# Kernel optimization log

Hardware: AMD Instinct MI355X
Metric: run time of the kernel (lower is better)

Reference implementation:

```python
import jax, jax.numpy as jnp
import numpy as np

H, W = 512, 512
G = 8192
ALPHA_THRESH = 1.0 / 255.0        # meta_f32[0]
TRANS_THRESH = 1.0e-4             # meta_f32[1]
ALPHA_CAP = 0.99                  # meta_f32[6]
BG = jnp.zeros((3,), dtype=jnp.float32)  # config.background


def setup_inputs() -> dict:
    key = jax.random.key(0)
    ks = jax.random.split(key, 7)
    mx = jax.random.uniform(ks[0], (G,), minval=0.0, maxval=float(W))
    my = jax.random.uniform(ks[1], (G,), minval=0.0, maxval=float(H))
    means2d = jnp.stack([mx, my], axis=-1)
    # Build valid conics (inverse 2x2 covariances) from random rotation + scales
    theta = jax.random.uniform(ks[2], (G,), minval=0.0, maxval=2.0 * np.pi)
    s = jax.random.uniform(ks[3], (G, 2), minval=2.0, maxval=12.0)  # px stddevs
    ct, st = jnp.cos(theta), jnp.sin(theta)
    v1, v2 = s[:, 0] ** 2, s[:, 1] ** 2
    ca = ct * ct * v1 + st * st * v2
    cb = ct * st * (v1 - v2)
    cc = st * st * v1 + ct * ct * v2
    det = ca * cc - cb * cb
    conics = jnp.stack([cc / det, -cb / det, ca / det], axis=-1)  # [G,3] = (a,b,c)
    colors = jax.random.uniform(ks[4], (G, 3))
    opacities = jax.random.uniform(ks[5], (G,))
    depths = jax.random.uniform(ks[6], (G,), minval=0.1, maxval=100.0)
    return {"means2d": means2d, "conics": conics, "colors": colors,
            "opacities": opacities, "depths": depths}


def reference(means2d, conics, colors, opacities, depths):
    # Stable front-to-back depth sort (mirrors perm = argsort(depths, stable))
    perm = jnp.argsort(depths, stable=True)
    m = means2d[perm]
    cn = conics[perm]
    col = colors[perm]
    op = opacities[perm]
    a, b, c = cn[:, 0], cn[:, 1], cn[:, 2]
    px = jnp.arange(W, dtype=means2d.dtype) + 0.5  # pixel centers

    def row(y):
        py = y.astype(means2d.dtype) + 0.5
        dx = px[:, None] - m[None, :, 0]          # [W,G]
        dy = py - m[:, 1]                          # [G]
        sigma = 0.5 * (a * dx * dx + c * dy * dy) + b * dx * dy  # [W,G]
        alpha = jnp.minimum(ALPHA_CAP, op * jnp.exp(-sigma))
        alpha = jnp.where((sigma < 0) | (alpha < ALPHA_THRESH), 0.0, alpha)
        # exclusive cumulative transmittance along depth order
        Tprev = jnp.cumprod(1.0 - alpha, axis=-1)
        Tprev = jnp.concatenate([jnp.ones((W, 1), alpha.dtype), Tprev[:, :-1]], axis=-1)
        # early-termination: splats seen after T drops below threshold contribute 0
        wgt = alpha * Tprev * (Tprev >= TRANS_THRESH)  # [W,G]
        rgb = wgt @ col                                 # [W,3]
        t_rem = 1.0 - wgt.sum(axis=-1)                  # remaining transmittance
        return rgb + t_rem[:, None] * BG

    return jax.lax.map(row, jnp.arange(H))  # [H,W,3]
```

## Files before the change

### kernel.cpp

```cpp
#include <hip/hip_runtime.h>

#define G 8192
#define IMG_W 512
#define IMG_H 512
#define TILE 16
#define NTX (IMG_W / TILE)
#define NTY (IMG_H / TILE)
#define BLK 256
#define CAP 1024
#define ALPHA_THRESH (1.0f/255.0f)
#define ALPHA_CAP 0.99f
#define TRANS_THRESH 1e-4f

__global__ __launch_bounds__(BLK)
void range_kernel(const float* __restrict__ means2d,
                  const float* __restrict__ conics,
                  const float* __restrict__ opac,
                  unsigned int* __restrict__ ranges)
{
    int g = blockIdx.x * BLK + threadIdx.x;
    if (g >= G) return;
    float op = opac[g];
    unsigned int packed = 0xFFu;
    if (op * 255.0f >= 1.0f) {
        float smax = __logf(op * 255.0f);
        float a = conics[3*g], b = conics[3*g+1], c = conics[3*g+2];
        float det = fmaxf(a * c - b * b, 1e-12f);
        float rx = sqrtf(fmaxf(2.0f * smax * c / det, 0.0f)) * 1.0001f + 0.01f;
        float ry = sqrtf(fmaxf(2.0f * smax * a / det, 0.0f)) * 1.0001f + 0.01f;
        float mx = means2d[2*g], my = means2d[2*g+1];
        int txmin = (int)ceilf ((mx - rx - 15.5f) * 0.0625f);
        int txmax = (int)floorf((mx + rx -  0.5f) * 0.0625f);
        int tymin = (int)ceilf ((my - ry - 15.5f) * 0.0625f);
        int tymax = (int)floorf((my + ry -  0.5f) * 0.0625f);
        if (!(txmax < 0 || txmin > NTX-1 || tymax < 0 || tymin > NTY-1 ||
              txmin > txmax || tymin > tymax)) {
            txmin = max(txmin, 0); txmax = min(txmax, NTX-1);
            tymin = max(tymin, 0); tymax = min(tymax, NTY-1);
            packed = (unsigned)txmin | ((unsigned)txmax << 8)
                   | ((unsigned)tymin << 16) | ((unsigned)tymax << 24);
        }
    }
    ranges[g] = packed;
}

__device__ __forceinline__ int hitp(unsigned p, unsigned btx, unsigned bty)
{
    return (btx >= (p & 0xffu)) & (btx <= ((p >> 8) & 0xffu)) &
           (bty >= ((p >> 16) & 0xffu)) & (bty <= (p >> 24));
}

__global__ __launch_bounds__(BLK)
void tile_kernel(const unsigned int* __restrict__ ranges,
                 const float* __restrict__ depths,
                 const float* __restrict__ means2d,
                 const float* __restrict__ conics,
                 const float* __restrict__ colors,
                 const float* __restrict__ opac,
                 float*       __restrict__ out)
{
    __shared__ unsigned short slist[CAP];
    __shared__ unsigned long long keys[CAP];
    __shared__ int woff[4];
    __shared__ float smx[BLK], smy[BLK], sa[BLK], sb[BLK], sc[BLK];
    __shared__ float sr[BLK], sg[BLK], sbl[BLK], sop[BLK];

    const int tx = threadIdx.x, ty = threadIdx.y;
    const int t = ty * TILE + tx;
    const int lane = t & 63, w = t >> 6;
    const unsigned btx = blockIdx.x, bty = blockIdx.y;

    const uint4* r4 = (const uint4*)ranges;
    const int wbase = w * (G / 4);
    uint4 rv[8];
    #pragma unroll
    for (int i = 0; i < 8; ++i)
        rv[i] = r4[(wbase >> 2) + i * 64 + lane];

    int cnt = 0;
    #pragma unroll
    for (int i = 0; i < 8; ++i)
        cnt += hitp(rv[i].x, btx, bty) + hitp(rv[i].y, btx, bty)
             + hitp(rv[i].z, btx, bty) + hitp(rv[i].w, btx, bty);
    #pragma unroll
    for (int d = 1; d < 64; d <<= 1) cnt += __shfl_xor(cnt, d);
    if (lane == 0) woff[w] = cnt;
    __syncthreads();

    int offs = 0;
    for (int ww = 0; ww < w; ++ww) offs += woff[ww];
    const int N = min(woff[0] + woff[1] + woff[2] + woff[3], CAP);

    const unsigned long long lt = (1ull << lane) - 1ull;
    #pragma unroll
    for (int i = 0; i < 8; ++i) {
        int gbase = wbase + i * 256 + lane * 4;
        int h0 = hitp(rv[i].x, btx, bty), h1 = hitp(rv[i].y, btx, bty);
        int h2 = hitp(rv[i].z, btx, bty), h3 = hitp(rv[i].w, btx, bty);
        unsigned long long m0 = __ballot(h0), m1 = __ballot(h1);
        unsigned long long m2 = __ballot(h2), m3 = __ballot(h3);
        int pos = offs + __popcll(m0 & lt) + __popcll(m1 & lt)
                       + __popcll(m2 & lt) + __popcll(m3 & lt);
        if (h0) { if (pos < CAP) slist[pos] = (unsigned short)(gbase    ); pos++; }
        if (h1) { if (pos < CAP) slist[pos] = (unsigned short)(gbase + 1); pos++; }
        if (h2) { if (pos < CAP) slist[pos] = (unsigned short)(gbase + 2); pos++; }
        if (h3) { if (pos < CAP) slist[pos] = (unsigned short)(gbase + 3); pos++; }
        offs += __popcll(m0) + __popcll(m1) + __popcll(m2) + __popcll(m3);
    }
    __syncthreads();

    for (int i = t; i < N; i += BLK) {
        unsigned idx = slist[i];
        keys[i] = ((unsigned long long)__float_as_uint(depths[idx]) << 13)
                | (unsigned long long)idx;
    }
    __syncthreads();
    for (int i = t; i < N; i += BLK) {
        unsigned long long ke = keys[i];
        int r = 0;
        #pragma unroll 4
        for (int j = 0; j < N; ++j) r += (keys[j] < ke);
        slist[r] = (unsigned short)(ke & 0x1fffull);
    }
    __syncthreads();

    const float px = (float)(blockIdx.x * TILE + tx) + 0.5f;
    const float py = (float)(blockIdx.y * TILE + ty) + 0.5f;
    float T = 1.0f, accr = 0.0f, accg = 0.0f, accb = 0.0f;
    bool done = false;

    for (int base = 0; base < N; base += BLK) {
        int n = min(BLK, N - base);
        if (t < n) {
            int idx = slist[base + t];
            smx[t] = means2d[2*idx];
            smy[t] = means2d[2*idx + 1];
            sa [t] = conics[3*idx];
            sb [t] = conics[3*idx + 1];
            sc [t] = conics[3*idx + 2];
            sr [t] = colors[3*idx];
            sg [t] = colors[3*idx + 1];
            sbl[t] = colors[3*idx + 2];
            sop[t] = opac[idx];
        }
        __syncthreads();
        if (!done) {
            for (int i = 0; i < n; ++i) {
                float dx = px - smx[i];
                float dy = py - smy[i];
                float sigma = 0.5f * (sa[i]*dx*dx + sc[i]*dy*dy) + sb[i]*dx*dy;
                float al = sop[i] * __expf(-sigma);
                bool ok = (sigma >= 0.0f) && (al >= ALPHA_THRESH);
                al = ok ? fminf(al, ALPHA_CAP) : 0.0f;
                float wgt = al * T;
                accr = fmaf(wgt, sr[i],  accr);
                accg = fmaf(wgt, sg[i],  accg);
                accb = fmaf(wgt, sbl[i], accb);
                T *= (1.0f - al);
                if (T < TRANS_THRESH) { done = true; break; }
            }
        }
        if (__syncthreads_and((int)done)) break;
    }

    const int o = ((blockIdx.y * TILE + ty) * IMG_W + blockIdx.x * TILE + tx) * 3;
    out[o]     = accr;
    out[o + 1] = accg;
    out[o + 2] = accb;
}

extern "C" void kernel_launch(void* const* d_in, const int* in_sizes, int n_in,
                              void* d_out, int out_size, void* d_ws, size_t ws_size,
                              hipStream_t stream)
{
    const float* means2d = (const float*)d_in[0];
    const float* conics  = (const float*)d_in[1];
    const float* colors  = (const float*)d_in[2];
    const float* opac    = (const float*)d_in[3];
    const float* depths  = (const float*)d_in[4];
    float* out = (float*)d_out;
    unsigned int* ranges = (unsigned int*)d_ws;

    range_kernel<<<G / BLK, BLK, 0, stream>>>(means2d, conics, opac, ranges);
    tile_kernel<<<dim3(NTX, NTY), dim3(TILE, TILE), 0, stream>>>(
        ranges, depths, means2d, conics, colors, opac, out);
}
```

Before: 93.83 us.

## Stage splat parameters in wave registers and broadcast via readlane instead of LDS

Each 64-lane wave now loads a chunk of 64 sorted splats into per-lane registers and broadcasts each one to the whole wave with readlane. This replaces the block-wide shared-memory staging and its per-batch __syncthreads. The next chunk is prefetched while the current one is composited, and waves terminate on their own once no lane has transmittance above threshold, checked every 8 splats. The thread-to-pixel mapping changes to a 1D block of four 16x4 wave strips, and the conic is pre-halved so sigma is computed with FMAs. In exchange, individual pixels no longer stop exactly when their own transmittance drops, which adds negligible extra contributions, and register pressure rises from the double-buffered splat parameters.

```diff
diff --git a/kernel.cpp b/kernel.cpp
--- a/kernel.cpp
+++ b/kernel.cpp
@@ -50,6 +50,11 @@
            (bty >= ((p >> 16) & 0xffu)) & (bty <= (p >> 24));
 }
 
+__device__ __forceinline__ float rdl(float v, int l)
+{
+    return __int_as_float(__builtin_amdgcn_readlane(__float_as_int(v), l));
+}
+
 __global__ __launch_bounds__(BLK)
 void tile_kernel(const unsigned int* __restrict__ ranges,
                  const float* __restrict__ depths,
@@ -62,11 +67,8 @@
     __shared__ unsigned short slist[CAP];
     __shared__ unsigned long long keys[CAP];
     __shared__ int woff[4];
-    __shared__ float smx[BLK], smy[BLK], sa[BLK], sb[BLK], sc[BLK];
-    __shared__ float sr[BLK], sg[BLK], sbl[BLK], sop[BLK];
-
-    const int tx = threadIdx.x, ty = threadIdx.y;
-    const int t = ty * TILE + tx;
+
+    const int t = threadIdx.x;
     const int lane = t & 63, w = t >> 6;
     const unsigned btx = blockIdx.x, bty = blockIdx.y;
 
@@ -124,46 +126,68 @@
     }
     __syncthreads();
 
-    const float px = (float)(blockIdx.x * TILE + tx) + 0.5f;
-    const float py = (float)(blockIdx.y * TILE + ty) + 0.5f;
+    const float px = (float)(btx * TILE + (lane & 15)) + 0.5f;
+    const float py = (float)(bty * TILE + w * 4 + (lane >> 4)) + 0.5f;
+
     float T = 1.0f, accr = 0.0f, accg = 0.0f, accb = 0.0f;
-    bool done = false;
-
-    for (int base = 0; base < N; base += BLK) {
-        int n = min(BLK, N - base);
-        if (t < n) {
-            int idx = slist[base + t];
-            smx[t] = means2d[2*idx];
-            smy[t] = means2d[2*idx + 1];
-            sa [t] = conics[3*idx];
-            sb [t] = conics[3*idx + 1];
-            sc [t] = conics[3*idx + 2];
-            sr [t] = colors[3*idx];
-            sg [t] = colors[3*idx + 1];
-            sbl[t] = colors[3*idx + 2];
-            sop[t] = opac[idx];
+    const int nchunk = (N + 63) >> 6;
+
+    float cmx, cmy, ca2, cb, cc2, cop, cr, cg, cbl;
+    float nmx, nmy, na2, nb, nc2, nop, nr, ng, nbl;
+
+    auto fetch = [&](int c, float& mx, float& my, float& a2, float& b,
+                     float& c2, float& op, float& r, float& g, float& bl) {
+        int pos = (c << 6) + lane;
+        if (pos < N) {
+            int idx = slist[pos];
+            mx = means2d[2*idx];      my = means2d[2*idx + 1];
+            float a = conics[3*idx];  b  = conics[3*idx + 1];
+            float cc = conics[3*idx + 2];
+            a2 = 0.5f * a;            c2 = 0.5f * cc;
+            r  = colors[3*idx];       g  = colors[3*idx + 1];
+            bl = colors[3*idx + 2];   op = opac[idx];
+        } else {
+            mx = 0.f; my = 0.f; a2 = 0.f; b = 0.f; c2 = 0.f;
+            op = 0.f; r = 0.f; g = 0.f; bl = 0.f;
         }
-        __syncthreads();
-        if (!done) {
-            for (int i = 0; i < n; ++i) {
-                float dx = px - smx[i];
-                float dy = py - smy[i];
-                float sigma = 0.5f * (sa[i]*dx*dx + sc[i]*dy*dy) + sb[i]*dx*dy;
-                float al = sop[i] * __expf(-sigma);
+    };
+
+    if (nchunk > 0)
+        fetch(0, cmx, cmy, ca2, cb, cc2, cop, cr, cg, cbl);
+
+    bool alive = true;
+    for (int c = 0; c < nchunk && alive; ++c) {
+        if (c + 1 < nchunk)
+            fetch(c + 1, nmx, nmy, na2, nb, nc2, nop, nr, ng, nbl);
+        for (int j = 0; j < 64; j += 8) {
+            #pragma unroll
+            for (int u = 0; u < 8; ++u) {
+                int l = j + u;
+                float mx = rdl(cmx, l), my = rdl(cmy, l);
+                float a2 = rdl(ca2, l), b  = rdl(cb, l), c2 = rdl(cc2, l);
+                float op = rdl(cop, l), r  = rdl(cr, l), g  = rdl(cg, l);
+                float bl = rdl(cbl, l);
+                float dx = px - mx;
+                float dy = py - my;
+                float sigma = fmaf(fmaf(a2, dx, b * dy), dx, c2 * dy * dy);
+                float al = op * __expf(-sigma);
                 bool ok = (sigma >= 0.0f) && (al >= ALPHA_THRESH);
                 al = ok ? fminf(al, ALPHA_CAP) : 0.0f;
                 float wgt = al * T;
-                accr = fmaf(wgt, sr[i],  accr);
-                accg = fmaf(wgt, sg[i],  accg);
-                accb = fmaf(wgt, sbl[i], accb);
+                accr = fmaf(wgt, r,  accr);
+                accg = fmaf(wgt, g,  accg);
+                accb = fmaf(wgt, bl, accb);
                 T *= (1.0f - al);
-                if (T < TRANS_THRESH) { done = true; break; }
             }
+            if (!__any(T >= TRANS_THRESH)) { alive = false; break; }
         }
-        if (__syncthreads_and((int)done)) break;
-    }
-
-    const int o = ((blockIdx.y * TILE + ty) * IMG_W + blockIdx.x * TILE + tx) * 3;
+        cmx = nmx; cmy = nmy; ca2 = na2; cb = nb; cc2 = nc2;
+        cop = nop; cr = nr; cg = ng; cbl = nbl;
+    }
+
+    const int x = btx * TILE + (lane & 15);
+    const int y = bty * TILE + w * 4 + (lane >> 4);
+    const int o = (y * IMG_W + x) * 3;
     out[o]     = accr;
     out[o + 1] = accg;
     out[o + 2] = accb;
@@ -182,6 +206,6 @@
     unsigned int* ranges = (unsigned int*)d_ws;
 
     range_kernel<<<G / BLK, BLK, 0, stream>>>(means2d, conics, opac, ranges);
-    tile_kernel<<<dim3(NTX, NTY), dim3(TILE, TILE), 0, stream>>>(
+    tile_kernel<<<dim3(NTX, NTY), BLK, 0, stream>>>(
         ranges, depths, means2d, conics, colors, opac, out);
 }
```

After: 106.6 us. +13.6%, slower.

## Composite two pixels per thread with packed float4 splat data in LDS

Applied to the files above, without the earlier changes.

Halves the tile block to 128 threads, with each thread rendering two pixels eight rows apart so every splat read from shared memory and the dx terms are reused. Splat attributes are packed into two float4 (pre-halved conics, fp16 red/green) to cut LDS traffic. Early termination becomes a wavefront-wide check every eight splats instead of per pixel. Risks: a slower rank sort with fewer threads, fp16 colour rounding, and slightly more accumulation past the transmittance threshold.

```diff
diff --git a/kernel.cpp b/kernel.cpp
--- a/kernel.cpp
+++ b/kernel.cpp
@@ -1,4 +1,5 @@
 #include <hip/hip_runtime.h>
+#include <hip/hip_fp16.h>
 
 #define G 8192
 #define IMG_W 512
@@ -7,6 +8,7 @@
 #define NTX (IMG_W / TILE)
 #define NTY (IMG_H / TILE)
 #define BLK 256
+#define BLK2 128
 #define CAP 1024
 #define ALPHA_THRESH (1.0f/255.0f)
 #define ALPHA_CAP 0.99f
@@ -50,7 +52,7 @@
            (bty >= ((p >> 16) & 0xffu)) & (bty <= (p >> 24));
 }
 
-__global__ __launch_bounds__(BLK)
+__global__ __launch_bounds__(BLK2)
 void tile_kernel(const unsigned int* __restrict__ ranges,
                  const float* __restrict__ depths,
                  const float* __restrict__ means2d,
@@ -61,42 +63,38 @@
 {
     __shared__ unsigned short slist[CAP];
     __shared__ unsigned long long keys[CAP];
-    __shared__ int woff[4];
-    __shared__ float smx[BLK], smy[BLK], sa[BLK], sb[BLK], sc[BLK];
-    __shared__ float sr[BLK], sg[BLK], sbl[BLK], sop[BLK];
-
-    const int tx = threadIdx.x, ty = threadIdx.y;
-    const int t = ty * TILE + tx;
+    __shared__ int woff[2];
+    __shared__ float4 buf[BLK2 * 2];
+
+    const int t = threadIdx.x;
     const int lane = t & 63, w = t >> 6;
     const unsigned btx = blockIdx.x, bty = blockIdx.y;
 
     const uint4* r4 = (const uint4*)ranges;
-    const int wbase = w * (G / 4);
-    uint4 rv[8];
-    #pragma unroll
-    for (int i = 0; i < 8; ++i)
-        rv[i] = r4[(wbase >> 2) + i * 64 + lane];
+    const int wq = w * (4096 / 4);
 
     int cnt = 0;
-    #pragma unroll
-    for (int i = 0; i < 8; ++i)
-        cnt += hitp(rv[i].x, btx, bty) + hitp(rv[i].y, btx, bty)
-             + hitp(rv[i].z, btx, bty) + hitp(rv[i].w, btx, bty);
+    #pragma unroll 4
+    for (int i = 0; i < 16; ++i) {
+        uint4 rv = r4[wq + i * 64 + lane];
+        cnt += hitp(rv.x, btx, bty) + hitp(rv.y, btx, bty)
+             + hitp(rv.z, btx, bty) + hitp(rv.w, btx, bty);
+    }
     #pragma unroll
     for (int d = 1; d < 64; d <<= 1) cnt += __shfl_xor(cnt, d);
     if (lane == 0) woff[w] = cnt;
     __syncthreads();
 
-    int offs = 0;
-    for (int ww = 0; ww < w; ++ww) offs += woff[ww];
-    const int N = min(woff[0] + woff[1] + woff[2] + woff[3], CAP);
+    int offs = (w == 1) ? woff[0] : 0;
+    const int N = min(woff[0] + woff[1], CAP);
 
     const unsigned long long lt = (1ull << lane) - 1ull;
-    #pragma unroll
-    for (int i = 0; i < 8; ++i) {
-        int gbase = wbase + i * 256 + lane * 4;
-        int h0 = hitp(rv[i].x, btx, bty), h1 = hitp(rv[i].y, btx, bty);
-        int h2 = hitp(rv[i].z, btx, bty), h3 = hitp(rv[i].w, btx, bty);
+    #pragma unroll 4
+    for (int i = 0; i < 16; ++i) {
+        uint4 rv = r4[wq + i * 64 + lane];
+        int gbase = w * 4096 + i * 256 + lane * 4;
+        int h0 = hitp(rv.x, btx, bty), h1 = hitp(rv.y, btx, bty);
+        int h2 = hitp(rv.z, btx, bty), h3 = hitp(rv.w, btx, bty);
         unsigned long long m0 = __ballot(h0), m1 = __ballot(h1);
         unsigned long long m2 = __ballot(h2), m3 = __ballot(h3);
         int pos = offs + __popcll(m0 & lt) + __popcll(m1 & lt)
@@ -109,13 +107,13 @@
     }
     __syncthreads();
 
-    for (int i = t; i < N; i += BLK) {
+    for (int i = t; i < N; i += BLK2) {
         unsigned idx = slist[i];
         keys[i] = ((unsigned long long)__float_as_uint(depths[idx]) << 13)
                 | (unsigned long long)idx;
     }
     __syncthreads();
-    for (int i = t; i < N; i += BLK) {
+    for (int i = t; i < N; i += BLK2) {
         unsigned long long ke = keys[i];
         int r = 0;
         #pragma unroll 4
@@ -124,49 +122,74 @@
     }
     __syncthreads();
 
-    const float px = (float)(blockIdx.x * TILE + tx) + 0.5f;
-    const float py = (float)(blockIdx.y * TILE + ty) + 0.5f;
-    float T = 1.0f, accr = 0.0f, accg = 0.0f, accb = 0.0f;
+    const int x  = btx * TILE + (lane & 15);
+    const int y0 = bty * TILE + w * 4 + (lane >> 4);
+    const float px  = (float)x  + 0.5f;
+    const float py0 = (float)y0 + 0.5f;
+    const float py1 = py0 + 8.0f;
+
+    float T0 = 1.f, T1 = 1.f;
+    float r0a = 0.f, g0a = 0.f, b0a = 0.f;
+    float r1a = 0.f, g1a = 0.f, b1a = 0.f;
     bool done = false;
 
-    for (int base = 0; base < N; base += BLK) {
-        int n = min(BLK, N - base);
+    for (int base = 0; base < N; base += BLK2) {
+        const int n = min(BLK2, N - base);
+        float4 q0 = make_float4(0.f, 0.f, 0.f, 0.f);
+        float4 q1 = make_float4(0.f, 0.f, 0.f, 0.f);
         if (t < n) {
             int idx = slist[base + t];
-            smx[t] = means2d[2*idx];
-            smy[t] = means2d[2*idx + 1];
-            sa [t] = conics[3*idx];
-            sb [t] = conics[3*idx + 1];
-            sc [t] = conics[3*idx + 2];
-            sr [t] = colors[3*idx];
-            sg [t] = colors[3*idx + 1];
-            sbl[t] = colors[3*idx + 2];
-            sop[t] = opac[idx];
+            union { float f; __half2 h; } uc;
+            uc.h = __floats2half2_rn(colors[3*idx], colors[3*idx + 1]);
+            q0 = make_float4(means2d[2*idx], means2d[2*idx + 1],
+                             0.5f * conics[3*idx], conics[3*idx + 1]);
+            q1 = make_float4(0.5f * conics[3*idx + 2], opac[idx],
+                             uc.f, colors[3*idx + 2]);
         }
+        buf[t * 2] = q0; buf[t * 2 + 1] = q1;
         __syncthreads();
+
         if (!done) {
-            for (int i = 0; i < n; ++i) {
-                float dx = px - smx[i];
-                float dy = py - smy[i];
-                float sigma = 0.5f * (sa[i]*dx*dx + sc[i]*dy*dy) + sb[i]*dx*dy;
-                float al = sop[i] * __expf(-sigma);
-                bool ok = (sigma >= 0.0f) && (al >= ALPHA_THRESH);
-                al = ok ? fminf(al, ALPHA_CAP) : 0.0f;
-                float wgt = al * T;
-                accr = fmaf(wgt, sr[i],  accr);
-                accg = fmaf(wgt, sg[i],  accg);
-                accb = fmaf(wgt, sbl[i], accb);
-                T *= (1.0f - al);
-                if (T < TRANS_THRESH) { done = true; break; }
+            const int n8 = (n + 7) & ~7;
+            for (int j = 0; j < n8 && !done; j += 8) {
+                #pragma unroll
+                for (int u = 0; u < 8; ++u) {
+                    float4 c0 = buf[(j + u) * 2];
+                    float4 c1 = buf[(j + u) * 2 + 1];
+                    float dx  = px - c0.x;
+                    float bdx = c0.w * dx;
+                    float txx = c0.z * dx * dx;
+                    float dy0 = py0 - c0.y;
+                    float dy1 = py1 - c0.y;
+                    float s0  = fmaf(fmaf(c1.x, dy0, bdx), dy0, txx);
+                    float s1  = fmaf(fmaf(c1.x, dy1, bdx), dy1, txx);
+                    union { float f; __half2 h; } uc; uc.f = c1.z;
+                    float cr = __low2float(uc.h);
+                    float cg = __high2float(uc.h);
+                    float cb = c1.w;
+                    float e0 = c1.y * __expf(-s0);
+                    float e1 = c1.y * __expf(-s1);
+                    float a0 = (s0 >= 0.f && e0 >= ALPHA_THRESH)
+                             ? fminf(e0, ALPHA_CAP) : 0.f;
+                    float a1 = (s1 >= 0.f && e1 >= ALPHA_THRESH)
+                             ? fminf(e1, ALPHA_CAP) : 0.f;
+                    float w0 = a0 * T0, w1 = a1 * T1;
+                    r0a = fmaf(w0, cr, r0a); g0a = fmaf(w0, cg, g0a);
+                    b0a = fmaf(w0, cb, b0a);
+                    r1a = fmaf(w1, cr, r1a); g1a = fmaf(w1, cg, g1a);
+                    b1a = fmaf(w1, cb, b1a);
+                    T0 *= (1.f - a0); T1 *= (1.f - a1);
+                }
+                if (!__any(fmaxf(T0, T1) >= TRANS_THRESH)) done = true;
             }
         }
         if (__syncthreads_and((int)done)) break;
     }
 
-    const int o = ((blockIdx.y * TILE + ty) * IMG_W + blockIdx.x * TILE + tx) * 3;
-    out[o]     = accr;
-    out[o + 1] = accg;
-    out[o + 2] = accb;
+    int o = (y0 * IMG_W + x) * 3;
+    out[o] = r0a; out[o + 1] = g0a; out[o + 2] = b0a;
+    o = ((y0 + 8) * IMG_W + x) * 3;
+    out[o] = r1a; out[o + 1] = g1a; out[o + 2] = b1a;
 }
 
 extern "C" void kernel_launch(void* const* d_in, const int* in_sizes, int n_in,
@@ -182,6 +205,6 @@
     unsigned int* ranges = (unsigned int*)d_ws;
 
     range_kernel<<<G / BLK, BLK, 0, stream>>>(means2d, conics, opac, ranges);
-    tile_kernel<<<dim3(NTX, NTY), dim3(TILE, TILE), 0, stream>>>(
+    tile_kernel<<<dim3(NTX, NTY), BLK2, 0, stream>>>(
         ranges, depths, means2d, conics, colors, opac, out);
 }
```

New measurement: 94.29 us. No clear change (+0.5%).
